# Kernel tuning notes

Measured on AMD Instinct MI355X. Metric: run time of the kernel, lower is better.

The kernel has to match this reference:

```python
import jax, jax.numpy as jnp
import numpy as np

TOPK = 2
EPS = float(np.finfo(np.float64).eps)


def setup_inputs() -> dict:
    key = jax.random.key(0)
    ks = jax.random.split(key, 6)
    B, D, E = 8192, 1024, 8
    x = jax.random.normal(ks[0], (B, D), dtype=jnp.float32)
    noise = jax.random.normal(ks[1], (B, E), dtype=jnp.float32)
    w_gate = jax.random.normal(ks[2], (D, E), dtype=jnp.float32) * 0.02
    w_noise = jax.random.normal(ks[3], (D, E), dtype=jnp.float32) * 0.02
    W_experts = jax.random.normal(ks[4], (E, D, D), dtype=jnp.float32) * 0.02
    b_experts = jax.random.normal(ks[5], (E, D), dtype=jnp.float32) * 0.02
    return {"x": x, "noise": noise, "w_gate": w_gate, "w_noise": w_noise,
            "W_experts": W_experts, "b_experts": b_experts}


def _gates(x, w_gate, w_noise, noise):
    # noisy top-k gating (Shazeer et al.)
    clean_logits = x @ w_gate                                  # [B, E]
    noise_stddev = jax.nn.softplus(x @ w_noise) + 0.01         # [B, E]
    logits = clean_logits + noise * noise_stddev               # [B, E]
    E = logits.shape[1]
    top_logits, top_idx = jax.lax.top_k(logits, min(TOPK + 1, E))
    top_k_logits = top_logits[:, :TOPK]
    top_k_idx = top_idx[:, :TOPK]
    top_k_gates = jax.nn.softmax(top_k_logits, axis=1)         # [B, k]
    B = logits.shape[0]
    gates = jnp.zeros_like(logits).at[jnp.arange(B)[:, None], top_k_idx].set(top_k_gates)
    return gates                                               # [B, E] sparse


def reference(x, noise, w_gate, w_noise, W_experts, b_experts):
    gates = _gates(x, w_gate, w_noise, noise)                  # [B, E]
    # dense equivalent of sort-based dispatch/combine: zero gates mask out
    # unselected experts, so the combined result is identical math.
    expert_out = jnp.einsum("bd,edh->beh", x, W_experts) + b_experts[None]  # [B, E, D]
    combined = jnp.einsum("be,beh->bh", gates, jnp.exp(expert_out))         # [B, D]
    combined = jnp.where(combined == 0, EPS, combined)
    return jnp.log(combined)
```

## Files before the change

### kernel.cpp

```cpp
#include <hip/hip_runtime.h>
#include <hip/hip_bf16.h>
#include <math.h>

#define B_ROWS 8192
#define DDIM   1024
#define NEXP   8

typedef __attribute__((ext_vector_type(8))) __bf16 bf16x8;
typedef __attribute__((ext_vector_type(4))) float  f32x4;

__device__ __forceinline__ unsigned short f2bf(float f) {
    unsigned u = __builtin_bit_cast(unsigned, f);
    u = (u + 0x7fffu + ((u >> 16) & 1u)) >> 16;
    return (unsigned short)u;
}

#define GLOAD_LDS16(gptr, lptr)                                                \
    __builtin_amdgcn_global_load_lds(                                          \
        (const __attribute__((address_space(1))) unsigned int*)(gptr),         \
        (__attribute__((address_space(3))) unsigned int*)(lptr), 16, 0, 0)

__global__ __launch_bounds__(256) void xconv_kernel(
    const float* __restrict__ x, __hip_bfloat16* __restrict__ xbf)
{
    int i = blockIdx.x * 256 + threadIdx.x;
    const int stride = gridDim.x * 256;
    const int n8 = B_ROWS * DDIM / 8;
    for (; i < n8; i += stride) {
        const float4 f0 = *(const float4*)(x + (size_t)i * 8);
        const float4 f1 = *(const float4*)(x + (size_t)i * 8 + 4);
        union { bf16x8 v; unsigned short u[8]; } pk;
        pk.u[0] = f2bf(f0.x); pk.u[1] = f2bf(f0.y); pk.u[2] = f2bf(f0.z); pk.u[3] = f2bf(f0.w);
        pk.u[4] = f2bf(f1.x); pk.u[5] = f2bf(f1.y); pk.u[6] = f2bf(f1.z); pk.u[7] = f2bf(f1.w);
        *(bf16x8*)((__hip_bfloat16*)xbf + (size_t)i * 8) = pk.v;
    }
}

__global__ __launch_bounds__(256) void wtrans_kernel(
    const float* __restrict__ W, __hip_bfloat16* __restrict__ Wt)
{
    const int e  = blockIdx.z;
    const int k0 = blockIdx.y * 64;
    const int n0 = blockIdx.x * 64;
    __shared__ float st[64][65];

    const int t = threadIdx.x;
    {
        const int kk = t >> 4;
        const int nn = (t & 15) * 4;
#pragma unroll
        for (int p = 0; p < 4; ++p) {
            const int k = p * 16 + kk;
            const float4 v = *(const float4*)(W + (size_t)e * DDIM * DDIM
                                                + (size_t)(k0 + k) * DDIM + n0 + nn);
            st[k][nn + 0] = v.x; st[k][nn + 1] = v.y;
            st[k][nn + 2] = v.z; st[k][nn + 3] = v.w;
        }
    }
    __syncthreads();
    {
        const int wave = t >> 6, lane = t & 63;
        const int nr = lane >> 3, kc = lane & 7;
#pragma unroll
        for (int p = 0; p < 2; ++p) {
            const int n = p * 32 + wave * 8 + nr;
            union { bf16x8 v; unsigned short u[8]; } pk;
#pragma unroll
            for (int j = 0; j < 8; ++j) pk.u[j] = f2bf(st[kc * 8 + j][n]);
            *(bf16x8*)((__hip_bfloat16*)Wt + (size_t)e * DDIM * DDIM
                        + (size_t)(n0 + n) * DDIM + k0 + kc * 8) = pk.v;
        }
    }
}

__global__ __launch_bounds__(256) void wprep_kernel(
    const float* __restrict__ wg, const float* __restrict__ wn, float* __restrict__ wtr)
{
    const int idx = blockIdx.x * 256 + threadIdx.x;
    if (idx < 16 * DDIM) {
        const int k8  = idx >> 7;
        const int rem = idx & 127;
        const int c   = rem >> 3;
        const int j   = rem & 7;
        const int k   = k8 * 8 + j;
        wtr[idx] = (c < 8) ? wg[k * NEXP + c] : wn[k * NEXP + (c - 8)];
    }
}

__global__ __launch_bounds__(256) void gating_kernel(
    const float* __restrict__ x, const float* __restrict__ noise,
    const float* __restrict__ wtr,
    int* __restrict__ counts, int* __restrict__ rowlist, float* __restrict__ gatelist)
{
    const int t = threadIdx.x;
    const int wave = t >> 6, lane = t & 63;
    const int ks = lane >> 5;
    const int rs = (lane >> 4) & 1;
    const int c  = lane & 15;
    const int row = blockIdx.x * 8 + wave * 2 + rs;

    const float* xr = x   + (size_t)row * DDIM + ks * 512;
    const float* wr = wtr + (size_t)ks * 8192 + c * 8;

    double a0 = 0, a1 = 0, a2 = 0, a3 = 0, a4 = 0, a5 = 0, a6 = 0, a7 = 0;
#pragma unroll 4
    for (int k8 = 0; k8 < 64; ++k8) {
        const float4 xv0 = *(const float4*)(xr + k8 * 8);
        const float4 xv1 = *(const float4*)(xr + k8 * 8 + 4);
        const float4 wv0 = *(const float4*)(wr + k8 * 128);
        const float4 wv1 = *(const float4*)(wr + k8 * 128 + 4);
        a0 += (double)(xv0.x * wv0.x);
        a1 += (double)(xv0.y * wv0.y);
        a2 += (double)(xv0.z * wv0.z);
        a3 += (double)(xv0.w * wv0.w);
        a4 += (double)(xv1.x * wv1.x);
        a5 += (double)(xv1.y * wv1.y);
        a6 += (double)(xv1.z * wv1.z);
        a7 += (double)(xv1.w * wv1.w);
    }
    double acc = ((a0 + a1) + (a2 + a3)) + ((a4 + a5) + (a6 + a7));

    acc += __shfl_xor(acc, 32);

    const double vnoise = __shfl_xor(acc, 8);

    double lgv = -1.0e300;
    if (c < 8) {
        const double z  = vnoise;
        const double sp = (z > 30.0) ? z : log1p(exp(z));
        lgv = acc + (double)noise[(size_t)row * NEXP + c] * (sp + 0.01);
    }

    double bv = lgv; int bi = c;
#pragma unroll
    for (int off = 1; off <= 4; off <<= 1) {
        const double ov = __shfl_xor(bv, off);
        const int    oi = __shfl_xor(bi, off);
        if (ov > bv || (ov == bv && oi < bi)) { bv = ov; bi = oi; }
    }
    double b2v = (c == bi) ? -1.0e300 : lgv; int b2i = c;
#pragma unroll
    for (int off = 1; off <= 4; off <<= 1) {
        const double ov = __shfl_xor(b2v, off);
        const int    oi = __shfl_xor(b2i, off);
        if (ov > b2v || (ov == b2v && oi < b2i)) { b2v = ov; b2i = oi; }
    }

    if ((lane & 47) == 0) {
        const double g0 = 1.0 / (1.0 + exp(b2v - bv));
        const double g1 = 1.0 - g0;
        int p0 = atomicAdd(&counts[bi], 1);
        rowlist [bi * B_ROWS + p0] = row;
        gatelist[bi * B_ROWS + p0] = (float)g0;
        int p1 = atomicAdd(&counts[b2i], 1);
        rowlist [b2i * B_ROWS + p1] = (int)((unsigned)row | 0x80000000u);
        gatelist[b2i * B_ROWS + p1] = (float)g1;
    }
}

__global__ __launch_bounds__(256) void moe_gemm_kernel(
    const __hip_bfloat16* __restrict__ xbf, const __hip_bfloat16* __restrict__ Wt,
    const float* __restrict__ bias,
    const int* __restrict__ counts, const int* __restrict__ rowlist,
    const float* __restrict__ gatelist, float* __restrict__ out, float* __restrict__ out2)
{
    const int nt = blockIdx.x;
    const int e  = blockIdx.y;
    const int mt = blockIdx.z;
    const int cnt  = counts[e];
    const int row0 = mt * 128;
    if (row0 >= cnt) return;

    __shared__ int   srow[128];
    __shared__ unsigned char srank[128];
    __shared__ float sgate[128];
    __shared__ __align__(16) unsigned char Alds[2][128 * 128];
    __shared__ __align__(16) unsigned char Blds[2][128 * 128];

    const int t = threadIdx.x;
    if (t < 128) {
        const int r = row0 + t;
        const unsigned er = (r < cnt) ? (unsigned)rowlist[e * B_ROWS + r] : 0u;
        srow[t]  = (int)(er & 0x7fffffffu);
        srank[t] = (unsigned char)(er >> 31);
        sgate[t] = (r < cnt) ? gatelist[e * B_ROWS + r] : 0.0f;
    }
    __syncthreads();

    const int wave = t >> 6, lane = t & 63;
    const int wr = wave >> 1, wc = wave & 1;
    const int l4 = lane >> 4, l16 = lane & 15;
    const int lrow  = lane >> 3;
    const int lchunk = (lane & 7) ^ lrow;

    const char* asrc[4]; const char* bsrc[4];
#pragma unroll
    for (int i = 0; i < 4; ++i) {
        const int r  = wave * 32 + i * 8 + lrow;
        asrc[i] = (const char*)xbf + 2 * ((size_t)srow[r] * DDIM + lchunk * 8);
        const int gn = nt * 128 + wave * 32 + i * 8 + lrow;
        bsrc[i] = (const char*)Wt  + 2 * ((size_t)e * DDIM * DDIM + (size_t)gn * DDIM + lchunk * 8);
    }

    f32x4 acc[4][4];
#pragma unroll
    for (int m = 0; m < 4; ++m)
#pragma unroll
        for (int n = 0; n < 4; ++n) acc[m][n] = (f32x4){0.f, 0.f, 0.f, 0.f};

#define STAGE(bufi, koff)                                                      \
    {                                                                          \
        _Pragma("unroll")                                                      \
        for (int i = 0; i < 4; ++i) {                                          \
            GLOAD_LDS16(asrc[i] + (koff), Alds[bufi] + (wave * 32 + i * 8) * 128); \
            GLOAD_LDS16(bsrc[i] + (koff), Blds[bufi] + (wave * 32 + i * 8) * 128); \
        }                                                                      \
    }

    STAGE(0, 0)
    asm volatile("s_waitcnt vmcnt(0)" ::: "memory");
    __builtin_amdgcn_s_barrier();

    int cur = 0;
    for (int kt = 0; kt < DDIM / 64; ++kt) {
        if (kt < DDIM / 64 - 1) STAGE(cur ^ 1, (kt + 1) * 128)

#pragma unroll
        for (int ks = 0; ks < 2; ++ks) {
            bf16x8 af[4], bfr[4];
#pragma unroll
            for (int m = 0; m < 4; ++m) {
                const int row = wr * 64 + m * 16 + l16;
                af[m] = *(const bf16x8*)(Alds[cur] + row * 128 + ((ks * 64 + l4 * 16) ^ ((row & 7) << 4)));
            }
#pragma unroll
            for (int n = 0; n < 4; ++n) {
                const int rn = wc * 64 + n * 16 + l16;
                bfr[n] = *(const bf16x8*)(Blds[cur] + rn * 128 + ((ks * 64 + l4 * 16) ^ ((rn & 7) << 4)));
            }
#pragma unroll
            for (int m = 0; m < 4; ++m)
#pragma unroll
                for (int n = 0; n < 4; ++n)
                    acc[m][n] = __builtin_amdgcn_mfma_f32_16x16x32_bf16(af[m], bfr[n], acc[m][n], 0, 0, 0);
        }

        asm volatile("s_waitcnt vmcnt(0)" ::: "memory");
        __builtin_amdgcn_s_barrier();
        cur ^= 1;
    }
#undef STAGE

#pragma unroll
    for (int m = 0; m < 4; ++m) {
#pragma unroll
        for (int n = 0; n < 4; ++n) {
#pragma unroll
            for (int j = 0; j < 4; ++j) {
                const int R = wr * 64 + m * 16 + l4 * 4 + j;
                if (row0 + R < cnt) {
                    const int   brow = srow[R];
                    const float g    = sgate[R];
                    const int   h    = nt * 128 + wc * 64 + n * 16 + l16;
                    const float v    = g * __expf(acc[m][n][j] + bias[e * DDIM + h]);
                    float* dst = srank[R] ? out2 : out;
                    dst[(size_t)brow * DDIM + h] = v;
                }
            }
        }
    }
}

__global__ __launch_bounds__(256) void logeps_kernel(
    float* __restrict__ o, const float* __restrict__ o2, int n4)
{
    const float EPSF = 2.220446049250313e-16f;
    int i = blockIdx.x * blockDim.x + threadIdx.x;
    const int stride = gridDim.x * blockDim.x;
    float4* p = (float4*)o;
    const float4* q = (const float4*)o2;
    for (; i < n4; i += stride) {
        float4 a = p[i];
        const float4 b = q[i];
        a.x += b.x; a.y += b.y; a.z += b.z; a.w += b.w;
        a.x = __logf(a.x == 0.0f ? EPSF : a.x);
        a.y = __logf(a.y == 0.0f ? EPSF : a.y);
        a.z = __logf(a.z == 0.0f ? EPSF : a.z);
        a.w = __logf(a.w == 0.0f ? EPSF : a.w);
        p[i] = a;
    }
}

extern "C" void kernel_launch(void* const* d_in, const int* in_sizes, int n_in,
                              void* d_out, int out_size, void* d_ws, size_t ws_size,
                              hipStream_t stream)
{
    const float* x       = (const float*)d_in[0];
    const float* noise   = (const float*)d_in[1];
    const float* w_gate  = (const float*)d_in[2];
    const float* w_noise = (const float*)d_in[3];
    const float* W       = (const float*)d_in[4];
    const float* bias    = (const float*)d_in[5];
    float* out = (float*)d_out;

    char* ws = (char*)d_ws;
    int*   counts   = (int*)ws;
    float* wtr      = (float*)(ws + 256);
    int*   rowlist  = (int*)(ws + 256 + 65536);
    float* gatelist = (float*)(ws + 256 + 65536 + NEXP * B_ROWS * 4);
    __hip_bfloat16* xbf = (__hip_bfloat16*)(ws + (1u << 20));
    __hip_bfloat16* Wt  = (__hip_bfloat16*)(ws + (1u << 20) + (16u << 20));
    float* out2 = (float*)(ws + (1u << 20) + (32u << 20));

    hipMemsetAsync(counts, 0, 64, stream);

    wprep_kernel<<<64, 256, 0, stream>>>(w_gate, w_noise, wtr);
    gating_kernel<<<B_ROWS / 8, 256, 0, stream>>>(x, noise, wtr,
                                                  counts, rowlist, gatelist);
    xconv_kernel<<<1024, 256, 0, stream>>>(x, xbf);
    wtrans_kernel<<<dim3(16, 16, NEXP), 256, 0, stream>>>(W, Wt);

    dim3 grid(NEXP , NEXP , B_ROWS / 128 );
    moe_gemm_kernel<<<grid, 256, 0, stream>>>(xbf, Wt, bias, counts, rowlist, gatelist,
                                              out, out2);

    logeps_kernel<<<2048, 256, 0, stream>>>(out, out2, out_size / 4);
}
```

Baseline: 381.3 us.

## Single-buffer MoE GEMM LDS tiles and batch gating loads

```diff
diff --git a/kernel.cpp b/kernel.cpp
--- a/kernel.cpp
+++ b/kernel.cpp
@@ -103,20 +103,27 @@
     const float* wr = wtr + (size_t)ks * 8192 + c * 8;
 
     double a0 = 0, a1 = 0, a2 = 0, a3 = 0, a4 = 0, a5 = 0, a6 = 0, a7 = 0;
-#pragma unroll 4
-    for (int k8 = 0; k8 < 64; ++k8) {
-        const float4 xv0 = *(const float4*)(xr + k8 * 8);
-        const float4 xv1 = *(const float4*)(xr + k8 * 8 + 4);
-        const float4 wv0 = *(const float4*)(wr + k8 * 128);
-        const float4 wv1 = *(const float4*)(wr + k8 * 128 + 4);
-        a0 += (double)(xv0.x * wv0.x);
-        a1 += (double)(xv0.y * wv0.y);
-        a2 += (double)(xv0.z * wv0.z);
-        a3 += (double)(xv0.w * wv0.w);
-        a4 += (double)(xv1.x * wv1.x);
-        a5 += (double)(xv1.y * wv1.y);
-        a6 += (double)(xv1.z * wv1.z);
-        a7 += (double)(xv1.w * wv1.w);
+    for (int ko = 0; ko < 16; ++ko) {
+        float4 xb[8], wb[8];
+#pragma unroll
+        for (int i = 0; i < 4; ++i) {
+            const int k8 = ko * 4 + i;
+            xb[2 * i]     = *(const float4*)(xr + k8 * 8);
+            xb[2 * i + 1] = *(const float4*)(xr + k8 * 8 + 4);
+            wb[2 * i]     = *(const float4*)(wr + k8 * 128);
+            wb[2 * i + 1] = *(const float4*)(wr + k8 * 128 + 4);
+        }
+#pragma unroll
+        for (int i = 0; i < 4; ++i) {
+            a0 += (double)(xb[2 * i].x     * wb[2 * i].x);
+            a1 += (double)(xb[2 * i].y     * wb[2 * i].y);
+            a2 += (double)(xb[2 * i].z     * wb[2 * i].z);
+            a3 += (double)(xb[2 * i].w     * wb[2 * i].w);
+            a4 += (double)(xb[2 * i + 1].x * wb[2 * i + 1].x);
+            a5 += (double)(xb[2 * i + 1].y * wb[2 * i + 1].y);
+            a6 += (double)(xb[2 * i + 1].z * wb[2 * i + 1].z);
+            a7 += (double)(xb[2 * i + 1].w * wb[2 * i + 1].w);
+        }
     }
     double acc = ((a0 + a1) + (a2 + a3)) + ((a4 + a5) + (a6 + a7));
 
@@ -174,8 +181,8 @@
     __shared__ int   srow[128];
     __shared__ unsigned char srank[128];
     __shared__ float sgate[128];
-    __shared__ __align__(16) unsigned char Alds[2][128 * 128];
-    __shared__ __align__(16) unsigned char Blds[2][128 * 128];
+    __shared__ __align__(16) unsigned char Alds[128 * 128];
+    __shared__ __align__(16) unsigned char Blds[128 * 128];
 
     const int t = threadIdx.x;
     if (t < 128) {
@@ -208,22 +215,15 @@
 #pragma unroll
         for (int n = 0; n < 4; ++n) acc[m][n] = (f32x4){0.f, 0.f, 0.f, 0.f};
 
-#define STAGE(bufi, koff)                                                      \
-    {                                                                          \
-        _Pragma("unroll")                                                      \
-        for (int i = 0; i < 4; ++i) {                                          \
-            GLOAD_LDS16(asrc[i] + (koff), Alds[bufi] + (wave * 32 + i * 8) * 128); \
-            GLOAD_LDS16(bsrc[i] + (koff), Blds[bufi] + (wave * 32 + i * 8) * 128); \
-        }                                                                      \
-    }
-
-    STAGE(0, 0)
-    asm volatile("s_waitcnt vmcnt(0)" ::: "memory");
-    __builtin_amdgcn_s_barrier();
-
-    int cur = 0;
     for (int kt = 0; kt < DDIM / 64; ++kt) {
-        if (kt < DDIM / 64 - 1) STAGE(cur ^ 1, (kt + 1) * 128)
+        const int koff = kt * 128;
+#pragma unroll
+        for (int i = 0; i < 4; ++i) {
+            GLOAD_LDS16(asrc[i] + koff, Alds + (wave * 32 + i * 8) * 128);
+            GLOAD_LDS16(bsrc[i] + koff, Blds + (wave * 32 + i * 8) * 128);
+        }
+        asm volatile("s_waitcnt vmcnt(0)" ::: "memory");
+        __syncthreads();
 
 #pragma unroll
         for (int ks = 0; ks < 2; ++ks) {
@@ -231,12 +231,12 @@
 #pragma unroll
             for (int m = 0; m < 4; ++m) {
                 const int row = wr * 64 + m * 16 + l16;
-                af[m] = *(const bf16x8*)(Alds[cur] + row * 128 + ((ks * 64 + l4 * 16) ^ ((row & 7) << 4)));
+                af[m] = *(const bf16x8*)(Alds + row * 128 + ((ks * 64 + l4 * 16) ^ ((row & 7) << 4)));
             }
 #pragma unroll
             for (int n = 0; n < 4; ++n) {
                 const int rn = wc * 64 + n * 16 + l16;
-                bfr[n] = *(const bf16x8*)(Blds[cur] + rn * 128 + ((ks * 64 + l4 * 16) ^ ((rn & 7) << 4)));
+                bfr[n] = *(const bf16x8*)(Blds + rn * 128 + ((ks * 64 + l4 * 16) ^ ((rn & 7) << 4)));
             }
 #pragma unroll
             for (int m = 0; m < 4; ++m)
@@ -244,12 +244,8 @@
                 for (int n = 0; n < 4; ++n)
                     acc[m][n] = __builtin_amdgcn_mfma_f32_16x16x32_bf16(af[m], bfr[n], acc[m][n], 0, 0, 0);
         }
-
-        asm volatile("s_waitcnt vmcnt(0)" ::: "memory");
-        __builtin_amdgcn_s_barrier();
-        cur ^= 1;
-    }
-#undef STAGE
+        __syncthreads();
+    }
 
 #pragma unroll
     for (int m = 0; m < 4; ++m) {
```

Measured after the change: 364.8 us. -4.3%, faster.
